# Kernel optimization log

Hardware: AMD Instinct MI355X
Metric: run time of the kernel (lower is better)

The kernel has to match this reference:

```python
import jax, jax.numpy as jnp
import numpy as np
from jax import lax

EPS = 1e-5

def _dsconv(x, dw, pw, g, b, m, v, relu):
    # x: [B,C,H,W]; dw: [C,1,3,3] depthwise; pw: [C,C,1,1] pointwise; eval-mode BN
    C = x.shape[1]
    y = lax.conv_general_dilated(x, dw, (1, 1), 'SAME', feature_group_count=C)
    y = lax.conv_general_dilated(y, pw, (1, 1), 'SAME')
    scale = (g * lax.rsqrt(v + EPS))[None, :, None, None]
    y = y * scale + (b - m * g * lax.rsqrt(v + EPS))[None, :, None, None]
    return jnp.maximum(y, 0.0) if relu else y

def _attention(x, wq, bq, wk, bk, wv, bv, gamma):
    b, c, h, w = x.shape
    n = h * w
    xf = x.reshape(b, c, n)                      # [B,C,N]
    q = jnp.einsum('oc,bcn->bon', wq, xf) + bq[None, :, None]   # [B,C/8,N]
    k = jnp.einsum('oc,bcn->bon', wk, xf) + bk[None, :, None]   # [B,C/8,N]
    v = jnp.einsum('oc,bcn->bon', wv, xf) + bv[None, :, None]   # [B,C,N]
    logits = jnp.einsum('bdm,bdn->bmn', q, k)    # q^T k, [B,N,N]
    attn = jax.nn.softmax(logits, axis=2)
    out = jnp.einsum('bcn,bmn->bcm', v, attn).reshape(b, c, h, w)
    return gamma[0] * out + x

def setup_inputs() -> dict:
    key = jax.random.key(0)
    ks = jax.random.split(key, 20)
    B, C, H, W = 64, 256, 32, 32
    C8 = C // 8
    rn = lambda k, s, sc: (jax.random.normal(k, s, dtype=jnp.float32) * sc)
    return {
        'x': rn(ks[0], (B, C, H, W), 1.0),
        'dw1': rn(ks[1], (C, 1, 3, 3), 0.2),
        'pw1': rn(ks[2], (C, C, 1, 1), 0.06),
        'bn1_g': jax.random.uniform(ks[3], (C,), jnp.float32, 0.5, 1.5),
        'bn1_b': rn(ks[4], (C,), 0.1),
        'bn1_m': rn(ks[5], (C,), 0.1),
        'bn1_v': jax.random.uniform(ks[6], (C,), jnp.float32, 0.5, 1.5),
        'dw2': rn(ks[7], (C, 1, 3, 3), 0.2),
        'pw2': rn(ks[8], (C, C, 1, 1), 0.06),
        'bn2_g': jax.random.uniform(ks[9], (C,), jnp.float32, 0.5, 1.5),
        'bn2_b': rn(ks[10], (C,), 0.1),
        'bn2_m': rn(ks[11], (C,), 0.1),
        'bn2_v': jax.random.uniform(ks[12], (C,), jnp.float32, 0.5, 1.5),
        'wq': rn(ks[13], (C8, C), 0.06),
        'bq': rn(ks[14], (C8,), 0.02),
        'wk': rn(ks[15], (C8, C), 0.06),
        'bk': rn(ks[16], (C8,), 0.02),
        'wv': rn(ks[17], (C, C), 0.06),
        'bv': rn(ks[18], (C,), 0.02),
        'gamma': rn(ks[19], (1,), 0.5),
    }

def reference(x, dw1, pw1, bn1_g, bn1_b, bn1_m, bn1_v,
              dw2, pw2, bn2_g, bn2_b, bn2_m, bn2_v,
              wq, bq, wk, bk, wv, bv, gamma):
    out = _dsconv(x, dw1, pw1, bn1_g, bn1_b, bn1_m, bn1_v, relu=True)
    out = _dsconv(out, dw2, pw2, bn2_g, bn2_b, bn2_m, bn2_v, relu=False)
    out = _attention(out + x, wq, bq, wk, bk, wv, bv, gamma)
    return jnp.maximum(out, 0.0)
```

## Files before the change

### kernel.cpp

```cpp
#include <hip/hip_runtime.h>
#include <cstdint>
#include <cstddef>

#define B_ 64
#define C_ 256
#define N_ 1024
#define LOG2E 1.4426950408889634f

typedef short v8s __attribute__((ext_vector_type(8)));
typedef float v4f __attribute__((ext_vector_type(4)));
typedef unsigned int u32;
typedef unsigned short u16;

#define VMCNT(N) asm volatile("s_waitcnt vmcnt(" #N ")" ::: "memory")
#define LGKM0 asm volatile("s_waitcnt lgkmcnt(0)" ::: "memory")
#define SBAR __builtin_amdgcn_s_barrier()
#define SCHEDB __builtin_amdgcn_sched_barrier(0)

__device__ __forceinline__ float bf2f(u16 u) {
  return __uint_as_float(((u32)u) << 16);
}
__device__ __forceinline__ u16 f2bf(float f) {
  u32 x = __float_as_uint(f);
  x += 0x7fffu + ((x >> 16) & 1u);
  return (u16)(x >> 16);
}
__device__ __forceinline__ u32 pack2(float a, float b) {
  return (u32)f2bf(a) | ((u32)f2bf(b) << 16);
}
__device__ __forceinline__ u32 cvtpk(float lo, float hi) {
  u32 r;
  asm("v_cvt_pk_bf16_f32 %0, %1, %2" : "=v"(r) : "v"(lo), "v"(hi));
  return r;
}

typedef __attribute__((address_space(3))) unsigned int lds_as_t;
typedef __attribute__((address_space(1))) const unsigned int glb_as_t;
__device__ __forceinline__ void ld_lds16(const u16* g, u16* l) {
  __builtin_amdgcn_global_load_lds((glb_as_t*)g, (lds_as_t*)l, 16, 0, 0);
}

__global__ __launch_bounds__(256) void prep(
    const float* __restrict__ g1, const float* __restrict__ b1,
    const float* __restrict__ m1, const float* __restrict__ v1,
    const float* __restrict__ g2, const float* __restrict__ b2,
    const float* __restrict__ m2, const float* __restrict__ v2,
    const float* __restrict__ wq, const float* __restrict__ bq,
    const float* __restrict__ wk, const float* __restrict__ bk,
    const float* __restrict__ wv, const float* __restrict__ bv,
    const float* __restrict__ pw1, const float* __restrict__ pw2,
    const float* __restrict__ dw1, const float* __restrict__ dw2,
    float* __restrict__ scale1, float* __restrict__ shift1,
    float* __restrict__ scale2, float* __restrict__ shift2,
    float* __restrict__ dwT1, float* __restrict__ dwT2,
    u16* __restrict__ pw1b, u16* __restrict__ pw2b, u16* __restrict__ wcatb,
    float* __restrict__ bcat) {
  const int gt = blockIdx.x * 256 + threadIdx.x;
  if (gt < 256) {
    float s1 = g1[gt] * rsqrtf(v1[gt] + 1e-5f);
    scale1[gt] = s1;
    shift1[gt] = b1[gt] - m1[gt] * s1;
    float s2 = g2[gt] * rsqrtf(v2[gt] + 1e-5f);
    scale2[gt] = s2;
    shift2[gt] = b2[gt] - m2[gt] * s2;
  }
  if (gt < 320)
    bcat[gt] = (gt < 32) ? bq[gt] * LOG2E
                         : (gt < 64) ? bk[gt - 32] : bv[gt - 64];
  if (gt < 2304) {
    dwT1[(gt % 9) * 256 + gt / 9] = dw1[gt];
    dwT2[(gt % 9) * 256 + gt / 9] = dw2[gt];
  }
  for (int e = gt; e < 65536; e += 16384) {
    pw1b[e] = f2bf(pw1[e]);
    pw2b[e] = f2bf(pw2[e]);
  }
  for (int e = gt; e < 81920; e += 16384) {
    const int o = e >> 8;
    float w = (o < 32) ? wq[e] * LOG2E
                       : (o < 64) ? wk[e - 8192] : wv[e - 16384];
    wcatb[e] = f2bf(w);
  }
}

__global__ __launch_bounds__(256) void transpose_x(const float* __restrict__ x,
                                                   u16* __restrict__ xt) {
  __shared__ float t[64][65];
  const int b = blockIdx.z, c0 = blockIdx.y * 64, n0 = blockIdx.x * 64;
  const float* xp = x + ((size_t)b * C_ + c0) * N_ + n0;
  const int tn = threadIdx.x & 63, tc = threadIdx.x >> 6;
#pragma unroll
  for (int i = 0; i < 16; ++i)
    t[tc + 4 * i][tn] = xp[(size_t)(tc + 4 * i) * N_ + tn];
  __syncthreads();
  u16* op = xt + ((size_t)b * N_ + n0) * C_ + c0;
  const int oc = threadIdx.x & 63, on = threadIdx.x >> 6;
#pragma unroll
  for (int i = 0; i < 16; ++i)
    op[(size_t)(on + 4 * i) * C_ + oc] = f2bf(t[oc][on + 4 * i]);
}

__global__ __launch_bounds__(256) void dw_nhwc(const u16* __restrict__ src,
                                               const float* __restrict__ wT,
                                               u16* __restrict__ dst) {
  __shared__ float wl[9][256];
  const int b = blockIdx.y;
  for (int e = threadIdx.x; e < 2304; e += 256) wl[e >> 8][e & 255] = wT[e];
  __syncthreads();
  const int pl = threadIdx.x >> 5, c0 = (threadIdx.x & 31) * 8;
  const int p = blockIdx.x * 8 + pl;
  const int h = p >> 5, wx = p & 31;
  const u16* sp = src + (size_t)b * N_ * C_;
  float acc[8] = {0.f, 0.f, 0.f, 0.f, 0.f, 0.f, 0.f, 0.f};
#pragma unroll
  for (int dh = -1; dh <= 1; ++dh) {
    const int hh = h + dh;
    if (hh < 0 || hh > 31) continue;
#pragma unroll
    for (int dx = -1; dx <= 1; ++dx) {
      const int ww = wx + dx;
      if (ww < 0 || ww > 31) continue;
      const int k = (dh + 1) * 3 + (dx + 1);
      const uint4 v = *(const uint4*)(sp + (size_t)(hh * 32 + ww) * C_ + c0);
      const u32 vv[4] = {v.x, v.y, v.z, v.w};
#pragma unroll
      for (int j = 0; j < 4; ++j) {
        acc[2 * j] += bf2f((u16)(vv[j] & 0xffffu)) * wl[k][c0 + 2 * j];
        acc[2 * j + 1] += bf2f((u16)(vv[j] >> 16)) * wl[k][c0 + 2 * j + 1];
      }
    }
  }
  uint4 o4;
  o4.x = pack2(acc[0], acc[1]);
  o4.y = pack2(acc[2], acc[3]);
  o4.z = pack2(acc[4], acc[5]);
  o4.w = pack2(acc[6], acc[7]);
  *(uint4*)(dst + ((size_t)b * N_ + p) * C_ + c0) = o4;
}

template <int EPI>
__global__ __launch_bounds__(256, 4) void gemm(
    const u16* __restrict__ X, const u16* __restrict__ W,
    const float* __restrict__ scale, const float* __restrict__ shift,
    const u16* __restrict__ resid, u16* __restrict__ Y, u16* __restrict__ Y2) {
  __shared__ u16 smem[17408];
  u16(*Ys)[136] = (u16(*)[136])smem;
  u16(*YsQ)[68] = (u16(*)[68])smem;

  const int tid = threadIdx.x;
  const int b = blockIdx.z;
  const int n0 = blockIdx.x * 128, o0 = blockIdx.y * 128;
  const int wid = tid >> 6, lane = tid & 63;
  const int wn = wid & 1, wo = wid >> 1;
  const int l15 = lane & 15, l4 = lane >> 4;
  const int r16 = lane >> 2, c16 = (lane & 3) * 8;

  v4f acc[4][4];
#pragma unroll
  for (int i = 0; i < 4; ++i)
#pragma unroll
    for (int j = 0; j < 4; ++j) acc[i][j] = v4f{0.f, 0.f, 0.f, 0.f};

  auto stage = [&](int kidx, int bufsel) {
    const int k0 = (kidx & 7) * 32;
    u16* Xd = smem + bufsel * 8192;
    u16* Wd = Xd + 4096;
#pragma unroll
    for (int g = 0; g < 2; ++g) {
      const int base = wid * 32 + g * 16;
      ld_lds16(X + ((size_t)b * N_ + n0 + base + r16) * C_ + k0 + c16,
               Xd + base * 32);
      int wr = o0 + base + r16;
      if (EPI == 2 && wr > 319) wr = 319;
      ld_lds16(W + (size_t)wr * C_ + k0 + c16, Wd + base * 32);
    }
  };

  stage(0, 0);
  stage(1, 1);

#pragma unroll
  for (int k = 0; k < 8; ++k) {
    const int cur = k & 1;
    if (k < 7) {
      VMCNT(4);
    } else {
      VMCNT(0);
    }
    SCHEDB;
    SBAR;
    const u16(*Xs)[32] = (const u16(*)[32])(smem + cur * 8192);
    const u16(*Ws)[32] = (const u16(*)[32])(smem + cur * 8192 + 4096);
    v8s af[4], bf4[4];
#pragma unroll
    for (int f = 0; f < 4; ++f) {
      if constexpr (EPI != 2) {
        af[f] = *(const v8s*)&Ws[wo * 64 + f * 16 + l15][l4 * 8];
        bf4[f] = *(const v8s*)&Xs[wn * 64 + f * 16 + l15][l4 * 8];
      } else {
        af[f] = *(const v8s*)&Xs[wn * 64 + f * 16 + l15][l4 * 8];
        bf4[f] = *(const v8s*)&Ws[wo * 64 + f * 16 + l15][l4 * 8];
      }
    }
#pragma unroll
    for (int i = 0; i < 4; ++i)
#pragma unroll
      for (int j = 0; j < 4; ++j)
        acc[i][j] = __builtin_amdgcn_mfma_f32_16x16x32_bf16(af[i], bf4[j],
                                                            acc[i][j], 0, 0, 0);
    LGKM0;
    SBAR;
    SCHEDB;
    if (k < 6) stage(k + 2, cur);
  }

  if constexpr (EPI != 2) {
#pragma unroll
    for (int i = 0; i < 4; ++i) {
      const int oL = wo * 64 + i * 16 + l4 * 4;
      const int o = o0 + oL;
      const float4 sc = *(const float4*)&scale[o];
      const float4 sh = *(const float4*)&shift[o];
#pragma unroll
      for (int j = 0; j < 4; ++j) {
        const int nL = wn * 64 + j * 16 + l15;
        float y0 = acc[i][j][0] * sc.x + sh.x;
        float y1 = acc[i][j][1] * sc.y + sh.y;
        float y2 = acc[i][j][2] * sc.z + sh.z;
        float y3 = acc[i][j][3] * sc.w + sh.w;
        if constexpr (EPI == 0) {
          y0 = fmaxf(y0, 0.f);
          y1 = fmaxf(y1, 0.f);
          y2 = fmaxf(y2, 0.f);
          y3 = fmaxf(y3, 0.f);
        } else {
          const uint2 rb =
              *(const uint2*)(resid + ((size_t)b * N_ + n0 + nL) * C_ + o);
          y0 += bf2f((u16)(rb.x & 0xffffu));
          y1 += bf2f((u16)(rb.x >> 16));
          y2 += bf2f((u16)(rb.y & 0xffffu));
          y3 += bf2f((u16)(rb.y >> 16));
        }
        uint2 st;
        st.x = pack2(y0, y1);
        st.y = pack2(y2, y3);
        *(uint2*)&Ys[nL][oL] = st;
      }
    }
    __syncthreads();
#pragma unroll
    for (int s = 0; s < 8; ++s) {
      const int nL = s * 16 + (tid >> 4);
      const int slot = tid & 15;
      const uint4 v = *(const uint4*)&Ys[nL][slot * 8];
      *(uint4*)&Y[((size_t)b * N_ + n0 + nL) * C_ + o0 + slot * 8] = v;
    }
  } else {
    float bj[4];
#pragma unroll
    for (int j = 0; j < 4; ++j) {
      int o = o0 + wo * 64 + j * 16 + l15;
      bj[j] = shift[o > 319 ? 319 : o];
    }
    if (o0 == 0 && wo == 0) {
#pragma unroll
      for (int i = 0; i < 4; ++i) {
        const int nL = wn * 64 + i * 16 + l4 * 4;
#pragma unroll
        for (int j = 0; j < 4; ++j) {
          const int oL = j * 16 + l15;
#pragma unroll
          for (int r = 0; r < 4; ++r)
            YsQ[nL + r][oL] = f2bf(acc[i][j][r] + bj[j]);
        }
      }
    } else {
#pragma unroll
      for (int i = 0; i < 4; ++i) {
        const int nL = wn * 64 + i * 16 + l4 * 4;
#pragma unroll
        for (int j = 0; j < 4; ++j) {
          const int oL = wo * 64 + j * 16 + l15;
          uint2 st;
          st.x = pack2(acc[i][j][0] + bj[j], acc[i][j][1] + bj[j]);
          st.y = pack2(acc[i][j][2] + bj[j], acc[i][j][3] + bj[j]);
          *(uint2*)&Ys[oL][nL] = st;
        }
      }
    }
    __syncthreads();
    if (o0 == 0) {
#pragma unroll
      for (int s = 0; s < 4; ++s) {
        const int e = s * 256 + tid;
        const int row = e >> 3, seg = e & 7;
        const uint4 v = *(const uint4*)&YsQ[row][seg * 8];
        *(uint4*)&Y[((size_t)b * N_ + n0 + row) * 64 + seg * 8] = v;
      }
#pragma unroll
      for (int s = 0; s < 4; ++s) {
        const int e = s * 256 + tid;
        const int oL = 64 + (e >> 4), slot = e & 15;
        const uint4 v = *(const uint4*)&Ys[oL][slot * 8];
        *(uint4*)&Y2[((size_t)b * C_ + oL - 64) * N_ + n0 + slot * 8] = v;
      }
    } else {
#pragma unroll
      for (int s = 0; s < 8; ++s) {
        const int oL = s * 16 + (tid >> 4);
        const int c = o0 + oL - 64;
        if (c < 256) {
          const int slot = tid & 15;
          const uint4 v = *(const uint4*)&Ys[oL][slot * 8];
          *(uint4*)&Y2[((size_t)b * C_ + c) * N_ + n0 + slot * 8] = v;
        }
      }
    }
  }
}

__global__ __launch_bounds__(256, 3) void flash(
    const u16* __restrict__ qk, const u16* __restrict__ vchw,
    const u16* __restrict__ abf, const float* __restrict__ gamma_p,
    float* __restrict__ out) {
  const int b = blockIdx.x;
  const int m0 = blockIdx.y * 64;
  const int tid = threadIdx.x, wid = tid >> 6, lane = tid & 63;
  const int l15 = lane & 15, l4 = lane >> 4;
  const int mw = m0 + wid * 16;
  const int cq = wid * 64;

  __shared__ u16 pool[25600];
  __shared__ float fscL[2][64];
  __shared__ float Sl[64];
  u16(*Vs)[64] = (u16(*)[64])pool;
  u16(*Pl)[64][72] = (u16(*)[64][72])(pool + 16384);
  u16* AB = pool;

  const u16* qkb = qk + (size_t)b * N_ * 64;
  const u16* vb = vchw + (size_t)b * C_ * N_;
  const v8s qf = *(const v8s*)&qkb[(size_t)(mw + l15) * 64 + l4 * 8];

  const int s_row = lane >> 3;
  const int s_j = (lane & 7) ^ (s_row & 7);

  v4f acc[4][4];
#pragma unroll
  for (int mf = 0; mf < 4; ++mf)
#pragma unroll
    for (int j = 0; j < 4; ++j) acc[mf][j] = v4f{0.f, 0.f, 0.f, 0.f};
  float M = -3e38f, S = 0.f;

  v8s kf[4];
#pragma unroll
  for (int f = 0; f < 4; ++f)
    kf[f] = *(const v8s*)&qkb[(size_t)(f * 16 + l15) * 64 + 32 + l4 * 8];
  VMCNT(0);
  SCHEDB;

  {
    v4f lt[4];
#pragma unroll
    for (int f = 0; f < 4; ++f)
      lt[f] = __builtin_amdgcn_mfma_f32_16x16x32_bf16(
          kf[f], qf, v4f{0.f, 0.f, 0.f, 0.f}, 0, 0, 0);
    float pmax = -3e38f;
#pragma unroll
    for (int f = 0; f < 4; ++f)
#pragma unroll
      for (int r = 0; r < 4; ++r) pmax = fmaxf(pmax, lt[f][r]);
    pmax = fmaxf(pmax, __shfl_xor(pmax, 16));
    pmax = fmaxf(pmax, __shfl_xor(pmax, 32));
    const float Mn = fmaxf(M, pmax);
    const float fsc = exp2f(M - Mn);
    float sum = 0.f;
#pragma unroll
    for (int f = 0; f < 4; ++f) {
      const float p0 = exp2f(lt[f][0] - Mn);
      const float p1 = exp2f(lt[f][1] - Mn);
      const float p2 = exp2f(lt[f][2] - Mn);
      const float p3 = exp2f(lt[f][3] - Mn);
      sum += (p0 + p1) + (p2 + p3);
      uint2 pw;
      pw.x = cvtpk(p0, p1);
      pw.y = cvtpk(p2, p3);
      *(uint2*)&Pl[0][wid * 16 + l15][f * 16 + l4 * 4] = pw;
    }
    S = S * fsc + sum;
    M = Mn;
    if (l4 == 0) fscL[0][wid * 16 + l15] = fsc;
#pragma unroll
    for (int f = 0; f < 4; ++f)
      kf[f] = *(const v8s*)&qkb[(size_t)(64 + f * 16 + l15) * 64 + 32 + l4 * 8];
    SCHEDB;
#pragma unroll
    for (int g = 0; g < 8; ++g) {
      const int base = cq + g * 8;
      ld_lds16(vb + (size_t)(base + s_row) * N_ + s_j * 8, &Vs[base][0]);
    }
    LGKM0;
    SBAR;
  }

  for (int t = 1; t < 16; ++t) {
    const int pb = (t - 1) & 1, cb = t & 1;
    VMCNT(8);
    SCHEDB;
    v4f lt[4];
#pragma unroll
    for (int f = 0; f < 4; ++f)
      lt[f] = __builtin_amdgcn_mfma_f32_16x16x32_bf16(
          kf[f], qf, v4f{0.f, 0.f, 0.f, 0.f}, 0, 0, 0);
    {
      v4f fr[4];
#pragma unroll
      for (int mf = 0; mf < 4; ++mf)
        fr[mf] = *(const v4f*)&fscL[pb][mf * 16 + l4 * 4];
#pragma unroll
      for (int mf = 0; mf < 4; ++mf)
#pragma unroll
        for (int j = 0; j < 4; ++j)
#pragma unroll
          for (int r = 0; r < 4; ++r) acc[mf][j][r] *= fr[mf][r];
    }
    VMCNT(0);
    SCHEDB;
    __builtin_amdgcn_s_setprio(1);
#pragma unroll
    for (int ks = 0; ks < 2; ++ks) {
      v8s pa[4];
#pragma unroll
      for (int mf = 0; mf < 4; ++mf)
        pa[mf] = *(const v8s*)&Pl[pb][mf * 16 + l15][ks * 32 + l4 * 8];
#pragma unroll
      for (int j = 0; j < 4; ++j) {
        const int col = 8 * (((ks * 4) + l4) ^ (l15 & 7));
        const v8s vf = *(const v8s*)&Vs[cq + j * 16 + l15][col];
#pragma unroll
        for (int mf = 0; mf < 4; ++mf)
          acc[mf][j] = __builtin_amdgcn_mfma_f32_16x16x32_bf16(
              pa[mf], vf, acc[mf][j], 0, 0, 0);
      }
    }
    __builtin_amdgcn_s_setprio(0);
    {
      float pmax = -3e38f;
#pragma unroll
      for (int f = 0; f < 4; ++f)
#pragma unroll
        for (int r = 0; r < 4; ++r) pmax = fmaxf(pmax, lt[f][r]);
      pmax = fmaxf(pmax, __shfl_xor(pmax, 16));
      pmax = fmaxf(pmax, __shfl_xor(pmax, 32));
      const float Mn = fmaxf(M, pmax);
      const float fsc = exp2f(M - Mn);
      float sum = 0.f;
#pragma unroll
      for (int f = 0; f < 4; ++f) {
        const float p0 = exp2f(lt[f][0] - Mn);
        const float p1 = exp2f(lt[f][1] - Mn);
        const float p2 = exp2f(lt[f][2] - Mn);
        const float p3 = exp2f(lt[f][3] - Mn);
        sum += (p0 + p1) + (p2 + p3);
        uint2 pw;
        pw.x = cvtpk(p0, p1);
        pw.y = cvtpk(p2, p3);
        *(uint2*)&Pl[cb][wid * 16 + l15][f * 16 + l4 * 4] = pw;
      }
      S = S * fsc + sum;
      M = Mn;
      if (l4 == 0) fscL[cb][wid * 16 + l15] = fsc;
    }
    {
      const int n1 = ((t + 1) & 15) * 64;
#pragma unroll
      for (int f = 0; f < 4; ++f)
        kf[f] =
            *(const v8s*)&qkb[(size_t)(n1 + f * 16 + l15) * 64 + 32 + l4 * 8];
    }
    SCHEDB;
    {
      const int n1 = t * 64;
#pragma unroll
      for (int g = 0; g < 8; ++g) {
        const int base = cq + g * 8;
        ld_lds16(vb + (size_t)(base + s_row) * N_ + n1 + s_j * 8, &Vs[base][0]);
      }
    }
    LGKM0;
    SBAR;
  }

  VMCNT(0);
  SCHEDB;
  {
    v4f fr[4];
#pragma unroll
    for (int mf = 0; mf < 4; ++mf)
      fr[mf] = *(const v4f*)&fscL[1][mf * 16 + l4 * 4];
#pragma unroll
    for (int mf = 0; mf < 4; ++mf)
#pragma unroll
      for (int j = 0; j < 4; ++j)
#pragma unroll
        for (int r = 0; r < 4; ++r) acc[mf][j][r] *= fr[mf][r];
  }
  __builtin_amdgcn_s_setprio(1);
#pragma unroll
  for (int ks = 0; ks < 2; ++ks) {
    v8s pa[4];
#pragma unroll
    for (int mf = 0; mf < 4; ++mf)
      pa[mf] = *(const v8s*)&Pl[1][mf * 16 + l15][ks * 32 + l4 * 8];
#pragma unroll
    for (int j = 0; j < 4; ++j) {
      const int col = 8 * (((ks * 4) + l4) ^ (l15 & 7));
      const v8s vf = *(const v8s*)&Vs[cq + j * 16 + l15][col];
#pragma unroll
      for (int mf = 0; mf < 4; ++mf)
        acc[mf][j] = __builtin_amdgcn_mfma_f32_16x16x32_bf16(
            pa[mf], vf, acc[mf][j], 0, 0, 0);
    }
  }
  __builtin_amdgcn_s_setprio(0);

  S += __shfl_xor(S, 16);
  S += __shfl_xor(S, 32);
  if (lane < 16) Sl[wid * 16 + lane] = 1.f / S;
  __syncthreads();

#pragma unroll
  for (int s = 0; s < 8; ++s) {
    const int e = s * 256 + tid;
    const int row = e >> 5, col = (e & 31) * 8;
    const uint4 v =
        *(const uint4*)(abf + ((size_t)b * N_ + m0 + row) * C_ + col);
    *(uint4*)&AB[row * 264 + col] = v;
  }
  float invv[4][4];
#pragma unroll
  for (int mf = 0; mf < 4; ++mf)
#pragma unroll
    for (int r = 0; r < 4; ++r) invv[mf][r] = Sl[mf * 16 + l4 * 4 + r];
  __syncthreads();

  const float gma = gamma_p[0];
#pragma unroll
  for (int mf = 0; mf < 4; ++mf) {
    const int mb = m0 + mf * 16 + l4 * 4;
#pragma unroll
    for (int j = 0; j < 4; ++j) {
      const int c = cq + j * 16 + l15;
      float4 y;
      float* yp = (float*)&y;
#pragma unroll
      for (int r = 0; r < 4; ++r) {
        const float av = bf2f(AB[(mf * 16 + l4 * 4 + r) * 264 + c]);
        yp[r] = fmaxf(gma * acc[mf][j][r] * invv[mf][r] + av, 0.f);
      }
      *(float4*)&out[((size_t)b * C_ + c) * N_ + mb] = y;
    }
  }
}

extern "C" void kernel_launch(void* const* d_in, const int* in_sizes, int n_in,
                              void* d_out, int out_size, void* d_ws,
                              size_t ws_size, hipStream_t stream) {
  const float* x = (const float*)d_in[0];
  const float* dw1 = (const float*)d_in[1];
  const float* pw1 = (const float*)d_in[2];
  const float* bn1g = (const float*)d_in[3];
  const float* bn1b = (const float*)d_in[4];
  const float* bn1m = (const float*)d_in[5];
  const float* bn1v = (const float*)d_in[6];
  const float* dw2 = (const float*)d_in[7];
  const float* pw2 = (const float*)d_in[8];
  const float* bn2g = (const float*)d_in[9];
  const float* bn2b = (const float*)d_in[10];
  const float* bn2m = (const float*)d_in[11];
  const float* bn2v = (const float*)d_in[12];
  const float* wq = (const float*)d_in[13];
  const float* bq = (const float*)d_in[14];
  const float* wk = (const float*)d_in[15];
  const float* bk = (const float*)d_in[16];
  const float* wv = (const float*)d_in[17];
  const float* bv = (const float*)d_in[18];
  const float* gamma = (const float*)d_in[19];
  float* out = (float*)d_out;

  char* ws = (char*)d_ws;
  size_t off = 0;
  auto alloc = [&](size_t bytes) {
    void* p = ws + off;
    off += (bytes + 255) & ~(size_t)255;
    return p;
  };
  const size_t NE = (size_t)B_ * N_ * C_;

  u16* bufA = (u16*)alloc(NE * 2);
  u16* bufB = (u16*)alloc(NE * 2);
  u16* bufC = (u16*)alloc(NE * 2);
  u16* abf = (u16*)alloc(NE * 2);
  float* scale1 = (float*)alloc(256 * 4);
  float* shift1 = (float*)alloc(256 * 4);
  float* scale2 = (float*)alloc(256 * 4);
  float* shift2 = (float*)alloc(256 * 4);
  float* dwT1 = (float*)alloc(2304 * 4);
  float* dwT2 = (float*)alloc(2304 * 4);
  u16* pw1b = (u16*)alloc(65536 * 2);
  u16* pw2b = (u16*)alloc(65536 * 2);
  u16* wcatb = (u16*)alloc(81920 * 2);
  float* bcat = (float*)alloc(384 * 4);

  u16* xt = bufA;
  u16* t1 = bufB;
  u16* y1 = bufC;
  u16* t2 = bufB;
  u16* qkbuf = bufC;
  u16* vchw = bufA;

  prep<<<64, 256, 0, stream>>>(bn1g, bn1b, bn1m, bn1v, bn2g, bn2b, bn2m, bn2v,
                               wq, bq, wk, bk, wv, bv, pw1, pw2, dw1, dw2,
                               scale1, shift1, scale2, shift2, dwT1, dwT2,
                               pw1b, pw2b, wcatb, bcat);
  transpose_x<<<dim3(16, 4, B_), 256, 0, stream>>>(x, xt);
  dw_nhwc<<<dim3(128, B_), 256, 0, stream>>>(xt, dwT1, t1);
  gemm<0><<<dim3(8, 2, B_), 256, 0, stream>>>(t1, pw1b, scale1, shift1,
                                              nullptr, y1, nullptr);
  dw_nhwc<<<dim3(128, B_), 256, 0, stream>>>(y1, dwT2, t2);
  gemm<1><<<dim3(8, 2, B_), 256, 0, stream>>>(t2, pw2b, scale2, shift2, xt,
                                              abf, nullptr);
  gemm<2><<<dim3(8, 3, B_), 256, 0, stream>>>(abf, wcatb, nullptr, bcat,
                                              nullptr, qkbuf, vchw);
  flash<<<dim3(64, 16), 256, 0, stream>>>(qkbuf, vchw, abf, gamma, out);
}
```

Measured before the change: 231.0 us.

## Load GEMM fragments directly to registers and skip online-softmax rescales lazily

```diff
diff --git a/kernel.cpp b/kernel.cpp
--- a/kernel.cpp
+++ b/kernel.cpp
@@ -139,7 +139,7 @@
 }
 
 template <int EPI>
-__global__ __launch_bounds__(256, 4) void gemm(
+__global__ __launch_bounds__(256, 2) void gemm(
     const u16* __restrict__ X, const u16* __restrict__ W,
     const float* __restrict__ scale, const float* __restrict__ shift,
     const u16* __restrict__ resid, u16* __restrict__ Y, u16* __restrict__ Y2) {
@@ -153,7 +153,16 @@
   const int wid = tid >> 6, lane = tid & 63;
   const int wn = wid & 1, wo = wid >> 1;
   const int l15 = lane & 15, l4 = lane >> 4;
-  const int r16 = lane >> 2, c16 = (lane & 3) * 8;
+
+  const u16* xp[4];
+  const u16* wp[4];
+#pragma unroll
+  for (int f = 0; f < 4; ++f) {
+    xp[f] = X + ((size_t)b * N_ + n0 + wn * 64 + f * 16 + l15) * C_ + l4 * 8;
+    int wr = o0 + wo * 64 + f * 16 + l15;
+    if (EPI == 2 && wr > 319) wr = 319;
+    wp[f] = W + (size_t)wr * C_ + l4 * 8;
+  }
 
   v4f acc[4][4];
 #pragma unroll
@@ -161,57 +170,34 @@
 #pragma unroll
     for (int j = 0; j < 4; ++j) acc[i][j] = v4f{0.f, 0.f, 0.f, 0.f};
 
-  auto stage = [&](int kidx, int bufsel) {
-    const int k0 = (kidx & 7) * 32;
-    u16* Xd = smem + bufsel * 8192;
-    u16* Wd = Xd + 4096;
-#pragma unroll
-    for (int g = 0; g < 2; ++g) {
-      const int base = wid * 32 + g * 16;
-      ld_lds16(X + ((size_t)b * N_ + n0 + base + r16) * C_ + k0 + c16,
-               Xd + base * 32);
-      int wr = o0 + base + r16;
-      if (EPI == 2 && wr > 319) wr = 319;
-      ld_lds16(W + (size_t)wr * C_ + k0 + c16, Wd + base * 32);
-    }
-  };
-
-  stage(0, 0);
-  stage(1, 1);
-
+  v8s wf[2][4], xf[2][4];
+#pragma unroll
+  for (int f = 0; f < 4; ++f) {
+    wf[0][f] = *(const v8s*)(wp[f]);
+    xf[0][f] = *(const v8s*)(xp[f]);
+  }
 #pragma unroll
   for (int k = 0; k < 8; ++k) {
-    const int cur = k & 1;
+    const int cur = k & 1, nxt = cur ^ 1;
     if (k < 7) {
-      VMCNT(4);
-    } else {
-      VMCNT(0);
-    }
-    SCHEDB;
-    SBAR;
-    const u16(*Xs)[32] = (const u16(*)[32])(smem + cur * 8192);
-    const u16(*Ws)[32] = (const u16(*)[32])(smem + cur * 8192 + 4096);
-    v8s af[4], bf4[4];
-#pragma unroll
-    for (int f = 0; f < 4; ++f) {
-      if constexpr (EPI != 2) {
-        af[f] = *(const v8s*)&Ws[wo * 64 + f * 16 + l15][l4 * 8];
-        bf4[f] = *(const v8s*)&Xs[wn * 64 + f * 16 + l15][l4 * 8];
-      } else {
-        af[f] = *(const v8s*)&Xs[wn * 64 + f * 16 + l15][l4 * 8];
-        bf4[f] = *(const v8s*)&Ws[wo * 64 + f * 16 + l15][l4 * 8];
+#pragma unroll
+      for (int f = 0; f < 4; ++f) {
+        wf[nxt][f] = *(const v8s*)(wp[f] + (k + 1) * 32);
+        xf[nxt][f] = *(const v8s*)(xp[f] + (k + 1) * 32);
       }
     }
 #pragma unroll
     for (int i = 0; i < 4; ++i)
 #pragma unroll
-      for (int j = 0; j < 4; ++j)
-        acc[i][j] = __builtin_amdgcn_mfma_f32_16x16x32_bf16(af[i], bf4[j],
-                                                            acc[i][j], 0, 0, 0);
-    LGKM0;
-    SBAR;
-    SCHEDB;
-    if (k < 6) stage(k + 2, cur);
+      for (int j = 0; j < 4; ++j) {
+        if constexpr (EPI != 2) {
+          acc[i][j] = __builtin_amdgcn_mfma_f32_16x16x32_bf16(
+              wf[cur][i], xf[cur][j], acc[i][j], 0, 0, 0);
+        } else {
+          acc[i][j] = __builtin_amdgcn_mfma_f32_16x16x32_bf16(
+              xf[cur][i], wf[cur][j], acc[i][j], 0, 0, 0);
+        }
+      }
   }
 
   if constexpr (EPI != 2) {
@@ -332,6 +318,7 @@
 
   __shared__ u16 pool[25600];
   __shared__ float fscL[2][64];
+  __shared__ u32 needF[2][4];
   __shared__ float Sl[64];
   u16(*Vs)[64] = (u16(*)[64])pool;
   u16(*Pl)[64][72] = (u16(*)[64][72])(pool + 16384);
@@ -389,6 +376,7 @@
     S = S * fsc + sum;
     M = Mn;
     if (l4 == 0) fscL[0][wid * 16 + l15] = fsc;
+    if (lane == 0) needF[0][wid] = 1u;
 #pragma unroll
     for (int f = 0; f < 4; ++f)
       kf[f] = *(const v8s*)&qkb[(size_t)(64 + f * 16 + l15) * 64 + 32 + l4 * 8];
@@ -412,16 +400,19 @@
       lt[f] = __builtin_amdgcn_mfma_f32_16x16x32_bf16(
           kf[f], qf, v4f{0.f, 0.f, 0.f, 0.f}, 0, 0, 0);
     {
-      v4f fr[4];
-#pragma unroll
-      for (int mf = 0; mf < 4; ++mf)
-        fr[mf] = *(const v4f*)&fscL[pb][mf * 16 + l4 * 4];
-#pragma unroll
-      for (int mf = 0; mf < 4; ++mf)
-#pragma unroll
-        for (int j = 0; j < 4; ++j)
-#pragma unroll
-          for (int r = 0; r < 4; ++r) acc[mf][j][r] *= fr[mf][r];
+      const uint4 nf = *(const uint4*)&needF[pb][0];
+      if (nf.x | nf.y | nf.z | nf.w) {
+        v4f fr[4];
+#pragma unroll
+        for (int mf = 0; mf < 4; ++mf)
+          fr[mf] = *(const v4f*)&fscL[pb][mf * 16 + l4 * 4];
+#pragma unroll
+        for (int mf = 0; mf < 4; ++mf)
+#pragma unroll
+          for (int j = 0; j < 4; ++j)
+#pragma unroll
+            for (int r = 0; r < 4; ++r) acc[mf][j][r] *= fr[mf][r];
+      }
     }
     VMCNT(0);
     SCHEDB;
@@ -451,15 +442,20 @@
         for (int r = 0; r < 4; ++r) pmax = fmaxf(pmax, lt[f][r]);
       pmax = fmaxf(pmax, __shfl_xor(pmax, 16));
       pmax = fmaxf(pmax, __shfl_xor(pmax, 32));
-      const float Mn = fmaxf(M, pmax);
-      const float fsc = exp2f(M - Mn);
+      const bool need = __any(pmax > M + 8.0f);
+      float fsc = 1.0f;
+      if (need) {
+        const float Mn = fmaxf(M, pmax);
+        fsc = exp2f(M - Mn);
+        M = Mn;
+      }
       float sum = 0.f;
 #pragma unroll
       for (int f = 0; f < 4; ++f) {
-        const float p0 = exp2f(lt[f][0] - Mn);
-        const float p1 = exp2f(lt[f][1] - Mn);
-        const float p2 = exp2f(lt[f][2] - Mn);
-        const float p3 = exp2f(lt[f][3] - Mn);
+        const float p0 = exp2f(lt[f][0] - M);
+        const float p1 = exp2f(lt[f][1] - M);
+        const float p2 = exp2f(lt[f][2] - M);
+        const float p3 = exp2f(lt[f][3] - M);
         sum += (p0 + p1) + (p2 + p3);
         uint2 pw;
         pw.x = cvtpk(p0, p1);
@@ -467,8 +463,8 @@
         *(uint2*)&Pl[cb][wid * 16 + l15][f * 16 + l4 * 4] = pw;
       }
       S = S * fsc + sum;
-      M = Mn;
       if (l4 == 0) fscL[cb][wid * 16 + l15] = fsc;
+      if (lane == 0) needF[cb][wid] = need ? 1u : 0u;
     }
     {
       const int n1 = ((t + 1) & 15) * 64;
@@ -493,16 +489,19 @@
   VMCNT(0);
   SCHEDB;
   {
-    v4f fr[4];
-#pragma unroll
-    for (int mf = 0; mf < 4; ++mf)
-      fr[mf] = *(const v4f*)&fscL[1][mf * 16 + l4 * 4];
-#pragma unroll
-    for (int mf = 0; mf < 4; ++mf)
-#pragma unroll
-      for (int j = 0; j < 4; ++j)
-#pragma unroll
-        for (int r = 0; r < 4; ++r) acc[mf][j][r] *= fr[mf][r];
+    const uint4 nf = *(const uint4*)&needF[1][0];
+    if (nf.x | nf.y | nf.z | nf.w) {
+      v4f fr[4];
+#pragma unroll
+      for (int mf = 0; mf < 4; ++mf)
+        fr[mf] = *(const v4f*)&fscL[1][mf * 16 + l4 * 4];
+#pragma unroll
+      for (int mf = 0; mf < 4; ++mf)
+#pragma unroll
+        for (int j = 0; j < 4; ++j)
+#pragma unroll
+          for (int r = 0; r < 4; ++r) acc[mf][j][r] *= fr[mf][r];
+    }
   }
   __builtin_amdgcn_s_setprio(1);
 #pragma unroll
```

Result: slower. 287.2 us (+24.3%).
